# Performance work log

Measured on AMD Instinct MI355X. Metric: run time of the kernel, lower is better.

## Reference

```python
import jax, jax.numpy as jnp
import numpy as np

B, S, IN = 4096, 2048, 8
H, LIN, A = 8, 4, 4

def _lstm_cell(x, h, c, Wih, Whh, bih, bhh):
    # torch gate order: i, f, g, o ; gates: [B, 4H]
    gates = x @ Wih.T + h @ Whh.T + bih + bhh
    i, f, g, o = jnp.split(gates, 4, axis=-1)
    i = jax.nn.sigmoid(i); f = jax.nn.sigmoid(f)
    g = jnp.tanh(g);       o = jax.nn.sigmoid(o)
    c = f * c + i * g
    h = o * jnp.tanh(c)
    return h, c

def setup_inputs() -> dict:
    key = jax.random.key(0)
    ks = jax.random.split(key, 20)
    seq = jax.random.normal(ks[0], (B, S, IN), dtype=jnp.float32)
    lengths = jax.random.randint(ks[1], (B,), 1, S + 1, dtype=jnp.int32)
    def w(k, shape, scale=0.1):
        return (jax.random.normal(k, shape, dtype=jnp.float32) * scale)
    return {
        "seq": seq, "lengths": lengths,
        # LSTM layer 0 (input 8 -> hidden 8)
        "Wih0": w(ks[2], (4 * H, IN)), "Whh0": w(ks[3], (4 * H, H)),
        "bih0": w(ks[4], (4 * H,)),   "bhh0": w(ks[5], (4 * H,)),
        # LSTM layer 1 (hidden 8 -> hidden 8)
        "Wih1": w(ks[6], (4 * H, H)), "Whh1": w(ks[7], (4 * H, H)),
        "bih1": w(ks[8], (4 * H,)),  "bhh1": w(ks[9], (4 * H,)),
        # heads
        "Wl": w(ks[10], (LIN, H)),  "bl": w(ks[11], (LIN,)),
        "Wv": w(ks[12], (1, LIN)),  "bv": jnp.zeros((1,), jnp.float32),
        "Wa": w(ks[13], (A, LIN)),  "ba": jnp.zeros((A,), jnp.float32),
        "log_std": jnp.zeros((1, A), jnp.float32),
    }

def reference(seq, lengths, Wih0, Whh0, bih0, bhh0, Wih1, Whh1, bih1, bhh1,
              Wl, bl, Wv, bv, Wa, ba, log_std):
    b = seq.shape[0]
    xs = jnp.transpose(seq, (1, 0, 2))  # [S, B, IN] time-major for scan
    z = jnp.zeros((b, H), seq.dtype)

    def step(carry, x_t):
        h0, c0, h1, c1 = carry
        h0, c0 = _lstm_cell(x_t, h0, c0, Wih0, Whh0, bih0, bhh0)
        h1, c1 = _lstm_cell(h0, h1, c1, Wih1, Whh1, bih1, bhh1)
        return (h0, c0, h1, c1), h1

    _, outs = jax.lax.scan(step, (z, z, z, z), xs)  # outs: [S, B, H]
    # packed-sequence semantics: take the last VALID output per sequence
    y = outs[lengths - 1, jnp.arange(b)]            # [B, H]
    feat = jnp.tanh(y @ Wl.T + bl)                  # [B, LIN]
    value = feat @ Wv.T + bv                        # [B, 1]
    action_mean = feat @ Wa.T + ba                  # [B, A]
    action_log_std = jnp.broadcast_to(log_std, action_mean.shape)
    action_std = jnp.exp(action_log_std)
    return value, action_mean, action_log_std, action_std
```

## Files before the change

kernel.cpp:

```cpp
#include <hip/hip_runtime.h>

#define B_ 4096
#define S_ 2048
#define CH 8

typedef float v2f __attribute__((ext_vector_type(2)));

__device__ __forceinline__ float rcp_(float x)  { return __builtin_amdgcn_rcpf(x); }
__device__ __forceinline__ float exp2_(float x) { return __builtin_amdgcn_exp2f(x); }
__device__ __forceinline__ float tanh_(float x) {
    return fmaf(-2.0f, rcp_(1.0f + exp2_(2.88539008f * x)), 1.0f);
}
template<int CTRL>
__device__ __forceinline__ float dppf(float x) {
    int v = __builtin_bit_cast(int, x);
    return __builtin_bit_cast(float,
        __builtin_amdgcn_update_dpp(v, v, CTRL, 0xF, 0xF, false));
}
#define ROR2f dppf<0x122>
__device__ __forceinline__ int dppi_ror2(int x) {
    return __builtin_amdgcn_update_dpp(x, x, 0x122, 0xF, 0xF, false);
}
__device__ __forceinline__ void ld8(const float* p, float* o) {
    float4 a = *(const float4*)p;
    float4 b = *(const float4*)(p + 4);
    o[0] = a.x; o[1] = a.y; o[2] = a.z; o[3] = a.w;
    o[4] = b.x; o[5] = b.y; o[6] = b.z; o[7] = b.w;
}

#define L2E 1.44269504f

__global__ __launch_bounds__(768) void lstm_main(
    const float* __restrict__ seq, const int* __restrict__ lengths,
    const float* __restrict__ Wih0, const float* __restrict__ Whh0,
    const float* __restrict__ bih0, const float* __restrict__ bhh0,
    const float* __restrict__ Wih1, const float* __restrict__ Whh1,
    const float* __restrict__ bih1, const float* __restrict__ bhh1,
    const float* __restrict__ Wl, const float* __restrict__ bl,
    const float* __restrict__ Wv, const float* __restrict__ bv,
    const float* __restrict__ Wa, const float* __restrict__ ba,
    const float* __restrict__ lstd, float* __restrict__ out)
{
    __shared__ float  ring0[2][CH][128];
    __shared__ float4 ringX[2][CH][16][8];
    __shared__ float4 ringY[2][CH][16][8];

    const int tid = threadIdx.x;
    const int wv  = tid >> 6;
    const int l   = tid & 63;
    const int p   = l & 1;
    const int j   = (l >> 1) & 7;
    const int s8  = (l >> 4) * 2 + p;

    const bool heavy = (wv % 3) == 0;
    int layer, sbase, s0 = 0;
    if (heavy) {
        const int hid = wv / 3;
        layer = hid >> 1;
        sbase = (hid & 1) * 8;
    } else {
        layer = (wv >= 7) ? 1 : 0;
        const int idx = (layer == 0) ? ((wv >= 4) ? (wv - 2) : (wv - 1))
                                     : ((wv >= 10) ? (wv - 8) : (wv - 7));
        sbase = (idx >> 1) * 8;
        s0    = (idx & 1) * 4;
    }
    const int sq = sbase + s8;
    const int b  = blockIdx.x * 16 + sq;

    const int probe = dppi_ror2(j);
    const int delta = (j - probe) & 7;

    v2f wA[8], wB[8];
    v2f biasA = (v2f){0.0f, 0.0f}, biasB = (v2f){0.0f, 0.0f};
    if (heavy) {
        const float* Whh = layer ? Whh1 : Whh0;
        int idx = j;
        #pragma unroll
        for (int k = 0; k < 8; ++k) {
            wA[k] = (v2f){ Whh[(j)      * 8 + idx] * -L2E,
                           Whh[(8 + j)  * 8 + idx] * -L2E };
            wB[k] = (v2f){ Whh[(16 + j) * 8 + idx] * (2.0f * L2E),
                           Whh[(24 + j) * 8 + idx] * -L2E };
            idx = (idx - delta) & 7;
        }
    } else {
        const float* Wih = layer ? Wih1 : Wih0;
        const float* bi  = layer ? bih1 : bih0;
        const float* bh  = layer ? bhh1 : bhh0;
        #pragma unroll
        for (int k = 0; k < 8; ++k) {
            wA[k] = (v2f){ Wih[(j)      * 8 + k] * -L2E,
                           Wih[(8 + j)  * 8 + k] * -L2E };
            wB[k] = (v2f){ Wih[(16 + j) * 8 + k] * (2.0f * L2E),
                           Wih[(24 + j) * 8 + k] * -L2E };
        }
        biasA = (v2f){ (bi[j]      + bh[j])      * -L2E,
                       (bi[8 + j]  + bh[8 + j])  * -L2E };
        biasB = (v2f){ (bi[16 + j] + bh[16 + j]) * (2.0f * L2E),
                       (bi[24 + j] + bh[24 + j]) * -L2E };
    }

    int m = lengths[blockIdx.x * 16 + (l & 15)];
    m = max(m, __shfl_xor(m, 1));
    m = max(m, __shfl_xor(m, 2));
    m = max(m, __shfl_xor(m, 4));
    m = max(m, __shfl_xor(m, 8));
    const int nch   = (m + CH - 1) / CH;
    const int lenm1 = lengths[b] - 1;

    float hq = 0.0f, cq = 0.0f, ysave = 0.0f;
    const float* xbase = seq + (size_t)b * S_ * 8;

    float xq[4][8];
    if (!heavy && layer == 0) {
        #pragma unroll
        for (int s = 0; s < 4; ++s) ld8(xbase + (size_t)(s0 + s) * 8, xq[s]);
    }
    if (heavy) __builtin_amdgcn_s_setprio(1);

    auto rstep = [&](v2f aA, v2f aB) {
        float rr = hq;
        #pragma unroll
        for (int q = 0; q < 8; ++q) {
            aA += wA[q] * (v2f){rr, rr};
            aB += wB[q] * (v2f){rr, rr};
            if (q < 7) rr = ROR2f(rr);
        }
        float Ei = exp2_(aA.x);
        float Ef = exp2_(aA.y);
        float Eg = exp2_(aB.x);
        float Eo = exp2_(aB.y);
        float sf  = rcp_(1.0f + Ef);
        float itg = (Eg - 1.0f) * rcp_((1.0f + Ei) * (1.0f + Eg));
        cq = fmaf(sf, cq, itg);
        float so = rcp_(1.0f + Eo);
        hq = so * tanh_(cq);
    };

    for (int k = 0; k <= nch + 2; ++k) {
        if (!heavy) {
            if (layer == 0) {
                if (k < nch) {
                    #pragma unroll
                    for (int s = 0; s < 4; ++s) {
                        v2f aA = biasA, aB = biasB;
                        #pragma unroll
                        for (int q = 0; q < 8; ++q) {
                            aA += wA[q] * (v2f){xq[s][q], xq[s][q]};
                            aB += wB[q] * (v2f){xq[s][q], xq[s][q]};
                        }
                        ringX[k & 1][s0 + s][sq][j] = make_float4(aA.x, aA.y, aB.x, aB.y);
                    }
                    if (k + 1 < nch) {
                        const int t0 = (k + 1) * CH + s0;
                        #pragma unroll
                        for (int s = 0; s < 4; ++s)
                            ld8(xbase + (size_t)(t0 + s) * 8, xq[s]);
                    }
                }
            } else {
                const int c = k - 2;
                if (c >= 0 && c < nch) {
                    #pragma unroll
                    for (int s = 0; s < 4; ++s) {
                        const float4 ha = *(const float4*)&ring0[c & 1][s0 + s][sq * 8];
                        const float4 hb = *(const float4*)&ring0[c & 1][s0 + s][sq * 8 + 4];
                        float hv[8] = {ha.x, ha.y, ha.z, ha.w, hb.x, hb.y, hb.z, hb.w};
                        v2f aA = biasA, aB = biasB;
                        #pragma unroll
                        for (int q = 0; q < 8; ++q) {
                            aA += wA[q] * (v2f){hv[q], hv[q]};
                            aB += wB[q] * (v2f){hv[q], hv[q]};
                        }
                        ringY[c & 1][s0 + s][sq][j] = make_float4(aA.x, aA.y, aB.x, aB.y);
                    }
                }
            }
        } else if (layer == 0) {
            const int c = k - 1;
            if (c >= 0 && c < nch) {
                float4 xg[CH];
                #pragma unroll
                for (int s = 0; s < CH; ++s) xg[s] = ringX[c & 1][s][sq][j];
                #pragma unroll
                for (int s = 0; s < CH; ++s) {
                    rstep((v2f){xg[s].x, xg[s].y}, (v2f){xg[s].z, xg[s].w});
                    ring0[c & 1][s][sq * 8 + j] = hq;
                }
            }
        } else {
            const int c = k - 3;
            if (c >= 0 && c < nch) {
                float4 yg[CH];
                #pragma unroll
                for (int s = 0; s < CH; ++s) yg[s] = ringY[c & 1][s][sq][j];
                const int u0 = c * CH;
                #pragma unroll
                for (int s = 0; s < CH; ++s) {
                    rstep((v2f){yg[s].x, yg[s].y}, (v2f){yg[s].z, yg[s].w});
                    ysave = (u0 + s == lenm1) ? hq : ysave;
                }
            }
        }
        __syncthreads();
    }

    if (heavy && layer == 1) {
        const int lbase = (l & 48) | p;
        float yv[8];
        #pragma unroll
        for (int k = 0; k < 8; ++k) yv[k] = __shfl(ysave, lbase + 2 * k);
        if (j == 0) {
            float feat[4];
            #pragma unroll
            for (int q = 0; q < 4; ++q) {
                float acc = bl[q];
                #pragma unroll
                for (int k = 0; k < 8; ++k) acc = fmaf(Wl[q * 8 + k], yv[k], acc);
                feat[q] = tanh_(acc);
            }
            float val = bv[0];
            #pragma unroll
            for (int q = 0; q < 4; ++q) val = fmaf(Wv[q], feat[q], val);
            out[b] = val;
            #pragma unroll
            for (int a = 0; a < 4; ++a) {
                float am = ba[a];
                #pragma unroll
                for (int q = 0; q < 4; ++q) am = fmaf(Wa[a * 4 + q], feat[q], am);
                out[4096  + b * 4 + a] = am;
                float ls = lstd[a];
                out[20480 + b * 4 + a] = ls;
                out[36864 + b * 4 + a] = exp2_(L2E * ls);
            }
        }
    }
}

extern "C" void kernel_launch(void* const* d_in, const int* in_sizes, int n_in,
                              void* d_out, int out_size, void* d_ws, size_t ws_size,
                              hipStream_t stream)
{
    const float* seq   = (const float*)d_in[0];
    const int* lengths = (const int*)d_in[1];
    const float* Wih0  = (const float*)d_in[2];
    const float* Whh0  = (const float*)d_in[3];
    const float* bih0  = (const float*)d_in[4];
    const float* bhh0  = (const float*)d_in[5];
    const float* Wih1  = (const float*)d_in[6];
    const float* Whh1  = (const float*)d_in[7];
    const float* bih1  = (const float*)d_in[8];
    const float* bhh1  = (const float*)d_in[9];
    const float* Wl    = (const float*)d_in[10];
    const float* bl    = (const float*)d_in[11];
    const float* Wv    = (const float*)d_in[12];
    const float* bv    = (const float*)d_in[13];
    const float* Wa    = (const float*)d_in[14];
    const float* ba    = (const float*)d_in[15];
    const float* lstd  = (const float*)d_in[16];

    lstm_main<<<B_ / 16, 768, 0, stream>>>(seq, lengths, Wih0, Whh0, bih0, bhh0,
                                           Wih1, Whh1, bih1, bhh1,
                                           Wl, bl, Wv, bv, Wa, ba, lstd,
                                           (float*)d_out);
}
```

Before: 647.8 us.

## Double chunk size, split recurrent dot-product chains, share one reciprocal per step

Raises the chunk length from 8 to 16 steps so the block-wide barrier runs half as often, and widens the helper waves' slices to 8 steps each. The recurrent matvec now builds all rotated hidden values up front with distinct DPP rotations and splits the accumulation into two independent chains. The four gate reciprocals are merged into a single rcp plus extra multiplies. Input prefetch for the next chunk is removed in favour of loading at the start of each chunk. In exchange it adds register and LDS pressure and load latency on the projection waves, and the merged reciprocal may change rounding or overflow behaviour.

```diff
diff --git a/kernel.cpp b/kernel.cpp
--- a/kernel.cpp
+++ b/kernel.cpp
@@ -2,7 +2,7 @@
 
 #define B_ 4096
 #define S_ 2048
-#define CH 8
+#define CH 16
 
 typedef float v2f __attribute__((ext_vector_type(2)));
 
@@ -17,7 +17,6 @@
     return __builtin_bit_cast(float,
         __builtin_amdgcn_update_dpp(v, v, CTRL, 0xF, 0xF, false));
 }
-#define ROR2f dppf<0x122>
 __device__ __forceinline__ int dppi_ror2(int x) {
     return __builtin_amdgcn_update_dpp(x, x, 0x122, 0xF, 0xF, false);
 }
@@ -63,7 +62,7 @@
         const int idx = (layer == 0) ? ((wv >= 4) ? (wv - 2) : (wv - 1))
                                      : ((wv >= 10) ? (wv - 8) : (wv - 7));
         sbase = (idx >> 1) * 8;
-        s0    = (idx & 1) * 4;
+        s0    = (idx & 1) * 8;
     }
     const int sq = sbase + s8;
     const int b  = blockIdx.x * 16 + sq;
@@ -112,29 +111,46 @@
     float hq = 0.0f, cq = 0.0f, ysave = 0.0f;
     const float* xbase = seq + (size_t)b * S_ * 8;
 
-    float xq[4][8];
-    if (!heavy && layer == 0) {
-        #pragma unroll
-        for (int s = 0; s < 4; ++s) ld8(xbase + (size_t)(s0 + s) * 8, xq[s]);
-    }
     if (heavy) __builtin_amdgcn_s_setprio(1);
 
     auto rstep = [&](v2f aA, v2f aB) {
-        float rr = hq;
-        #pragma unroll
-        for (int q = 0; q < 8; ++q) {
-            aA += wA[q] * (v2f){rr, rr};
-            aB += wB[q] * (v2f){rr, rr};
-            if (q < 7) rr = ROR2f(rr);
-        }
-        float Ei = exp2_(aA.x);
-        float Ef = exp2_(aA.y);
-        float Eg = exp2_(aB.x);
-        float Eo = exp2_(aB.y);
-        float sf  = rcp_(1.0f + Ef);
-        float itg = (Eg - 1.0f) * rcp_((1.0f + Ei) * (1.0f + Eg));
+        const float r0 = hq;
+        const float r1 = dppf<0x122>(hq);
+        const float r2 = dppf<0x124>(hq);
+        const float r3 = dppf<0x126>(hq);
+        const float r4 = dppf<0x128>(hq);
+        const float r5 = dppf<0x12A>(hq);
+        const float r6 = dppf<0x12C>(hq);
+        const float r7 = dppf<0x12E>(hq);
+        v2f aA1, aB1;
+        aA  += wA[0] * (v2f){r0, r0};
+        aB  += wB[0] * (v2f){r0, r0};
+        aA1  = wA[4] * (v2f){r4, r4};
+        aB1  = wB[4] * (v2f){r4, r4};
+        aA  += wA[1] * (v2f){r1, r1};
+        aB  += wB[1] * (v2f){r1, r1};
+        aA1 += wA[5] * (v2f){r5, r5};
+        aB1 += wB[5] * (v2f){r5, r5};
+        aA  += wA[2] * (v2f){r2, r2};
+        aB  += wB[2] * (v2f){r2, r2};
+        aA1 += wA[6] * (v2f){r6, r6};
+        aB1 += wB[6] * (v2f){r6, r6};
+        aA  += wA[3] * (v2f){r3, r3};
+        aB  += wB[3] * (v2f){r3, r3};
+        aA1 += wA[7] * (v2f){r7, r7};
+        aB1 += wB[7] * (v2f){r7, r7};
+        aA += aA1; aB += aB1;
+        float Ei = exp2_(aA.x), Ef = exp2_(aA.y);
+        float Eg = exp2_(aB.x), Eo = exp2_(aB.y);
+        float pi = 1.0f + Ei, pf = 1.0f + Ef;
+        float pg = 1.0f + Eg, po = 1.0f + Eo;
+        float P  = pi * pg;
+        float T  = P * pf;
+        float R  = rcp_(T * po);
+        float sf  = (R * P) * po;
+        float itg = ((Eg - 1.0f) * (R * pf)) * po;
         cq = fmaf(sf, cq, itg);
-        float so = rcp_(1.0f + Eo);
+        float so = R * T;
         hq = so * tanh_(cq);
     };
 
@@ -142,28 +158,27 @@
         if (!heavy) {
             if (layer == 0) {
                 if (k < nch) {
+                    const int t0 = k * CH + s0;
+                    float xv[8][8];
                     #pragma unroll
-                    for (int s = 0; s < 4; ++s) {
+                    for (int s = 0; s < 8; ++s)
+                        ld8(xbase + (size_t)(t0 + s) * 8, xv[s]);
+                    #pragma unroll
+                    for (int s = 0; s < 8; ++s) {
                         v2f aA = biasA, aB = biasB;
                         #pragma unroll
                         for (int q = 0; q < 8; ++q) {
-                            aA += wA[q] * (v2f){xq[s][q], xq[s][q]};
-                            aB += wB[q] * (v2f){xq[s][q], xq[s][q]};
+                            aA += wA[q] * (v2f){xv[s][q], xv[s][q]};
+                            aB += wB[q] * (v2f){xv[s][q], xv[s][q]};
                         }
                         ringX[k & 1][s0 + s][sq][j] = make_float4(aA.x, aA.y, aB.x, aB.y);
-                    }
-                    if (k + 1 < nch) {
-                        const int t0 = (k + 1) * CH + s0;
-                        #pragma unroll
-                        for (int s = 0; s < 4; ++s)
-                            ld8(xbase + (size_t)(t0 + s) * 8, xq[s]);
                     }
                 }
             } else {
                 const int c = k - 2;
                 if (c >= 0 && c < nch) {
                     #pragma unroll
-                    for (int s = 0; s < 4; ++s) {
+                    for (int s = 0; s < 8; ++s) {
                         const float4 ha = *(const float4*)&ring0[c & 1][s0 + s][sq * 8];
                         const float4 hb = *(const float4*)&ring0[c & 1][s0 + s][sq * 8 + 4];
                         float hv[8] = {ha.x, ha.y, ha.z, ha.w, hb.x, hb.y, hb.z, hb.w};
@@ -183,10 +198,11 @@
                 float4 xg[CH];
                 #pragma unroll
                 for (int s = 0; s < CH; ++s) xg[s] = ringX[c & 1][s][sq][j];
+                float* r0p = &ring0[c & 1][0][sq * 8 + j];
                 #pragma unroll
                 for (int s = 0; s < CH; ++s) {
                     rstep((v2f){xg[s].x, xg[s].y}, (v2f){xg[s].z, xg[s].w});
-                    ring0[c & 1][s][sq * 8 + j] = hq;
+                    r0p[s * 128] = hq;
                 }
             }
         } else {
```

Result: no change. 646.8 us (-0.2%).
